# Kernel tuning notes

Measured on AMD Instinct MI355X. Metric: run time of the kernel, lower is better.

## Reference

```python
import jax, jax.numpy as jnp
import numpy as np

N_NODES = 50000
N_EDGES = 800000
D_IN = 128
D_HID = 512
D_OUT = 128


def setup_inputs() -> dict:
    key = jax.random.key(0)
    k1, k2, k3, k4, k5, k6 = jax.random.split(key, 6)
    input_matrix = jax.random.normal(k1, (N_NODES, D_IN), dtype=jnp.float32)
    adjacency_coo_matrix = jax.random.randint(k2, (2, N_EDGES), 0, N_NODES, dtype=jnp.int64)
    # fc net params (torch Linear: y = x @ W.T + b); store W already transposed [D_IN, D_HID]
    lim_fc = 1.0 / np.sqrt(D_IN)
    fc_w = jax.random.uniform(k3, (D_IN, D_HID), dtype=jnp.float32, minval=-lim_fc, maxval=lim_fc)
    fc_b = jax.random.uniform(k4, (D_HID,), dtype=jnp.float32, minval=-lim_fc, maxval=lim_fc)
    # xavier_uniform for [D_IN + D_HID, D_OUT]
    lim_w = np.sqrt(6.0 / (D_IN + D_HID + D_OUT))
    weights_matrix = jax.random.uniform(k5, (D_IN + D_HID, D_OUT), dtype=jnp.float32, minval=-lim_w, maxval=lim_w)
    return {
        "input_matrix": input_matrix,
        "fc_w": fc_w,
        "fc_b": fc_b,
        "weights_matrix": weights_matrix,
        "adjacency_coo_matrix": adjacency_coo_matrix,
    }


def reference(input_matrix, fc_w, fc_b, weights_matrix, adjacency_coo_matrix):
    edge_src, edge_trg = adjacency_coo_matrix[0], adjacency_coo_matrix[1]
    n_nodes = input_matrix.shape[0]
    # gather neighbor features: [E, D_IN]
    neighbors = input_matrix[edge_trg]
    # per-edge MLP + relu: [E, D_HID]
    neighbors_repr = jax.nn.relu(neighbors @ fc_w + fc_b)
    # scatter-max reduce into per-node slots; relu outputs are >= 0, and
    # empty segments map to 0 (matching torch_scatter zero-fill), so clamp at 0
    agg = jax.ops.segment_max(neighbors_repr, edge_src, num_segments=n_nodes)
    agg = jnp.maximum(agg, 0.0)
    concat = jnp.concatenate([input_matrix, agg], axis=1)  # [N, D_IN + D_HID]
    return concat @ weights_matrix  # [N, D_OUT]
```

## Files before the change

kernel.cpp:

```cpp
#include <hip/hip_runtime.h>
#include <hip/hip_bf16.h>

#define N_NODES 50000
#define N_EDGES 800000
#define D_IN 128
#define D_HID 512
#define D_OUT 128
#define CAT_DIM 640
#define CAP 64

typedef __attribute__((ext_vector_type(8))) short short8;
typedef __attribute__((ext_vector_type(4))) float floatx4;

__device__ __forceinline__ unsigned short f2bf(float f) {
    unsigned u = __float_as_uint(f);
    unsigned r = u + 0x7fffu + ((u >> 16) & 1u);
    return (unsigned short)(r >> 16);
}

__device__ __forceinline__ void cvt8(const float* __restrict__ src, unsigned short* o) {
    float4 v0 = *(const float4*)src;
    float4 v1 = *(const float4*)(src + 4);
    o[0] = f2bf(v0.x); o[1] = f2bf(v0.y); o[2] = f2bf(v0.z); o[3] = f2bf(v0.w);
    o[4] = f2bf(v1.x); o[5] = f2bf(v1.y); o[6] = f2bf(v1.z); o[7] = f2bf(v1.w);
}


#define P0_FCW_BLOCKS 256
#define P0_W2_BLOCKS  320
#define P0_DEG_BLOCKS 196
#define P0_BLOCKS (P0_FCW_BLOCKS + P0_W2_BLOCKS + P0_DEG_BLOCKS)

__global__ void prep0_kernel(const float* __restrict__ fcW, const float* __restrict__ Wm,
                             unsigned short* __restrict__ fcwT,
                             unsigned short* __restrict__ WT,
                             int* __restrict__ deg) {
    int b = blockIdx.x, tid = threadIdx.x;
    if (b < P0_FCW_BLOCKS) {
        int idx = b * 256 + tid;
        int k = idx >> 9;
        int n = idx & (D_HID - 1);
        fcwT[n * D_IN + k] = f2bf(fcW[idx]);
        return;
    }
    b -= P0_FCW_BLOCKS;
    if (b < P0_W2_BLOCKS) {
        int idx = b * 256 + tid;
        int k = idx >> 7;
        int n = idx & (D_OUT - 1);
        WT[n * CAT_DIM + k] = f2bf(Wm[idx]);
        return;
    }
    b -= P0_W2_BLOCKS;
    int idx = b * 256 + tid;
    if (idx < N_NODES) deg[idx] = 0;
}


__device__ __forceinline__ void hist_edges(const int* __restrict__ adj, int s, int e0,
                                           int* __restrict__ deg, int* __restrict__ edge_list) {
    int src0, src1, trg0, trg1;
    if (s == 2) {
        int4 vs = *(const int4*)(adj + 2 * (size_t)e0);
        int4 vt = *(const int4*)(adj + 2 * ((size_t)N_EDGES + e0));
        src0 = vs.x; src1 = vs.z;
        trg0 = vt.x; trg1 = vt.z;
    } else {
        int2 vs = *(const int2*)(adj + e0);
        int2 vt = *(const int2*)(adj + N_EDGES + e0);
        src0 = vs.x; src1 = vs.y;
        trg0 = vt.x; trg1 = vt.y;
    }
    int p0 = atomicAdd(&deg[src0], 1);
    if (p0 < CAP) edge_list[src0 * CAP + p0] = trg0;
    int p1 = atomicAdd(&deg[src1], 1);
    if (p1 < CAP) edge_list[src1 * CAP + p1] = trg1;
}


#define HIST_BLOCKS 1563
#define GEMM_MT      782
#define G1_PAD 8

__global__ __launch_bounds__(256)
void mid_kernel(const int* __restrict__ adj,
                int* __restrict__ deg, int* __restrict__ edge_list,
                const float* __restrict__ X,
                const unsigned short* __restrict__ fcwT,
                const float* __restrict__ fcb,
                unsigned short* __restrict__ F) {
    int tid = threadIdx.x;
    if (blockIdx.x < HIST_BLOCKS) {
        int v = adj[2 * (tid & 63) + 1];
        int s = (__ballot(v != 0) == 0ULL) ? 2 : 1;
        int e0 = (blockIdx.x * 256 + tid) * 2;
        if (e0 < N_EDGES) hist_edges(adj, s, e0, deg, edge_list);
        return;
    }
    __shared__ unsigned short As[64][D_IN + G1_PAD];
    __shared__ unsigned short Bs[64][D_IN + G1_PAD];
    int lane = tid & 63, w = tid >> 6;
    int bm = (blockIdx.x - HIST_BLOCKS) * 64;
    {
        int r = tid >> 4;
        int c = (tid & 15) * 8;
        #pragma unroll
        for (int p = 0; p < 4; ++p) {
            int row = r + p * 16;
            int gr = bm + row;
            unsigned short o[8] = {0, 0, 0, 0, 0, 0, 0, 0};
            if (gr < N_NODES) cvt8(X + (size_t)gr * D_IN + c, o);
            *(uint4*)(&As[row][c]) = *(const uint4*)o;
        }
    }
    int wm = (w >> 1) * 32, wn = (w & 1) * 32;
    int q = lane >> 4, l16 = lane & 15;
    for (int nc = 0; nc < 8; ++nc) {
        {
            int r = tid >> 4;
            int c = (tid & 15) * 8;
            #pragma unroll
            for (int p = 0; p < 4; ++p) {
                int row = r + p * 16;
                *(uint4*)(&Bs[row][c]) =
                    *(const uint4*)(fcwT + (size_t)(nc * 64 + row) * D_IN + c);
            }
        }
        __syncthreads();
        floatx4 acc[2][2] = {};
        #pragma unroll
        for (int ks = 0; ks < 4; ++ks) {
            short8 af[2], bf[2];
            #pragma unroll
            for (int mi = 0; mi < 2; ++mi)
                af[mi] = *(const short8*)(&As[wm + mi * 16 + l16][ks * 32 + q * 8]);
            #pragma unroll
            for (int ni = 0; ni < 2; ++ni)
                bf[ni] = *(const short8*)(&Bs[wn + ni * 16 + l16][ks * 32 + q * 8]);
            #pragma unroll
            for (int mi = 0; mi < 2; ++mi)
                #pragma unroll
                for (int ni = 0; ni < 2; ++ni)
                    acc[mi][ni] = __builtin_amdgcn_mfma_f32_16x16x32_bf16(af[mi], bf[ni], acc[mi][ni], 0, 0, 0);
        }
        #pragma unroll
        for (int mi = 0; mi < 2; ++mi)
            #pragma unroll
            for (int ni = 0; ni < 2; ++ni)
                #pragma unroll
                for (int r = 0; r < 4; ++r) {
                    int row = bm + wm + mi * 16 + q * 4 + r;
                    int col = nc * 64 + wn + ni * 16 + l16;
                    if (row < N_NODES) {
                        float v = fmaxf(acc[mi][ni][r] + fcb[col], 0.0f);
                        F[(size_t)row * D_HID + col] = f2bf(v);
                    }
                }
        __syncthreads();
    }
}


__device__ __forceinline__ void fmax_bf16x8(float* acc, const uint4& p) {
    const unsigned* a = (const unsigned*)&p;
    #pragma unroll
    for (int j = 0; j < 4; ++j) {
        unsigned u = a[j];
        acc[2 * j]     = fmaxf(acc[2 * j],     __uint_as_float(u << 16));
        acc[2 * j + 1] = fmaxf(acc[2 * j + 1], __uint_as_float(u & 0xffff0000u));
    }
}

__global__ __launch_bounds__(256)
void aggregate_kernel(const unsigned short* __restrict__ F,
                      const int* __restrict__ deg,
                      const int* __restrict__ edge_list,
                      unsigned short* __restrict__ agg) {
    int gw = (blockIdx.x * 256 + threadIdx.x) >> 6;
    if (gw >= N_NODES) return;
    int lane = threadIdx.x & 63;
    int d = deg[gw];
    d = d < CAP ? d : CAP;
    const int* el = edge_list + gw * CAP;
    float acc[8] = {0.f, 0.f, 0.f, 0.f, 0.f, 0.f, 0.f, 0.f};
    int i = 0;
    for (; i + 2 <= d; i += 2) {
        int t0 = el[i], t1 = el[i + 1];
        uint4 p0 = *(const uint4*)(F + (size_t)t0 * D_HID + lane * 8);
        uint4 p1 = *(const uint4*)(F + (size_t)t1 * D_HID + lane * 8);
        fmax_bf16x8(acc, p0);
        fmax_bf16x8(acc, p1);
    }
    if (i < d) {
        uint4 p0 = *(const uint4*)(F + (size_t)el[i] * D_HID + lane * 8);
        fmax_bf16x8(acc, p0);
    }
    unsigned out[4];
    #pragma unroll
    for (int j = 0; j < 4; ++j) {
        unsigned lo = __float_as_uint(acc[2 * j]) >> 16;
        unsigned hi = __float_as_uint(acc[2 * j + 1]) & 0xffff0000u;
        out[j] = lo | hi;
    }
    *(uint4*)(agg + (size_t)gw * D_HID + lane * 8) = *(uint4*)out;
}


#define GPAD 8

__global__ __launch_bounds__(256)
void gemm2_kernel(const float* __restrict__ X,
                  const unsigned short* __restrict__ agg,
                  const unsigned short* __restrict__ WT,
                  float* __restrict__ out) {
    __shared__ unsigned short As[64][64 + GPAD];
    __shared__ unsigned short Bs[128][64 + GPAD];
    int tid = threadIdx.x;
    int lane = tid & 63, w = tid >> 6;
    int wm = (w >> 1) * 32, wn = (w & 1) * 64;
    int q = lane >> 4, l16 = lane & 15;
    int bm = blockIdx.x * 64;
    floatx4 acc[2][4] = {};
    int ra = tid >> 2;
    int ca = (tid & 3) * 8;
    int rb = tid >> 1;
    int cb = (tid & 1) * 8;

    for (int k0 = 0; k0 < CAT_DIM; k0 += 64) {
        {
            int gr = bm + ra;
            #pragma unroll
            for (int p = 0; p < 2; ++p) {
                int col = k0 + ca + p * 32;
                unsigned short o[8] = {0, 0, 0, 0, 0, 0, 0, 0};
                if (gr < N_NODES) {
                    if (col < D_IN) cvt8(X + (size_t)gr * D_IN + col, o);
                    else *(uint4*)o = *(const uint4*)(agg + (size_t)gr * D_HID + (col - D_IN));
                }
                *(uint4*)(&As[ra][ca + p * 32]) = *(const uint4*)o;
            }
        }
        {
            const unsigned short* bp = WT + (size_t)rb * CAT_DIM + k0 + cb;
            #pragma unroll
            for (int p = 0; p < 4; ++p)
                *(uint4*)(&Bs[rb][cb + p * 16]) = *(const uint4*)(bp + p * 16);
        }
        __syncthreads();
        #pragma unroll
        for (int ks = 0; ks < 2; ++ks) {
            short8 af[2], bf[4];
            #pragma unroll
            for (int mi = 0; mi < 2; ++mi)
                af[mi] = *(const short8*)(&As[wm + mi * 16 + l16][ks * 32 + q * 8]);
            #pragma unroll
            for (int ni = 0; ni < 4; ++ni)
                bf[ni] = *(const short8*)(&Bs[wn + ni * 16 + l16][ks * 32 + q * 8]);
            #pragma unroll
            for (int mi = 0; mi < 2; ++mi)
                #pragma unroll
                for (int ni = 0; ni < 4; ++ni)
                    acc[mi][ni] = __builtin_amdgcn_mfma_f32_16x16x32_bf16(af[mi], bf[ni], acc[mi][ni], 0, 0, 0);
        }
        __syncthreads();
    }

    #pragma unroll
    for (int mi = 0; mi < 2; ++mi)
        #pragma unroll
        for (int ni = 0; ni < 4; ++ni)
            #pragma unroll
            for (int r = 0; r < 4; ++r) {
                int row = bm + wm + mi * 16 + q * 4 + r;
                int col = wn + ni * 16 + l16;
                if (row < N_NODES)
                    out[(size_t)row * D_OUT + col] = acc[mi][ni][r];
            }
}


extern "C" void kernel_launch(void* const* d_in, const int* in_sizes, int n_in,
                              void* d_out, int out_size, void* d_ws, size_t ws_size,
                              hipStream_t stream) {
    const float* X    = (const float*)d_in[0];
    const float* fc_w = (const float*)d_in[1];
    const float* fc_b = (const float*)d_in[2];
    const float* Wm   = (const float*)d_in[3];
    const int*   adj  = (const int*)d_in[4];
    float* outp = (float*)d_out;

    char* ws = (char*)d_ws;
    size_t off = 0;
    auto alloc = [&](size_t bytes) -> void* {
        void* p = ws + off;
        off = (off + bytes + 255) & ~(size_t)255;
        return p;
    };
    unsigned short* agg    = (unsigned short*)alloc((size_t)N_NODES * D_HID * 2);
    unsigned short* F      = (unsigned short*)alloc((size_t)N_NODES * D_HID * 2);
    unsigned short* fcwT   = (unsigned short*)alloc((size_t)D_HID * D_IN * 2);
    unsigned short* WT     = (unsigned short*)alloc((size_t)D_OUT * CAT_DIM * 2);
    int* deg       = (int*)alloc((size_t)N_NODES * 4);
    int* edge_list = (int*)alloc((size_t)N_NODES * CAP * 4);

    prep0_kernel<<<P0_BLOCKS, 256, 0, stream>>>(fc_w, Wm, fcwT, WT, deg);
    mid_kernel<<<HIST_BLOCKS + GEMM_MT, 256, 0, stream>>>(adj, deg, edge_list,
                                                          X, fcwT, fc_b, F);
    aggregate_kernel<<<(N_NODES * 64) / 256, 256, 0, stream>>>(F, deg, edge_list, agg);
    gemm2_kernel<<<GEMM_MT, 256, 0, stream>>>(X, agg, WT, outp);
}
```

Baseline: 290.0 us.

## Split GEMM1 into 64x128 output tiles across four times more blocks

The per-node MLP GEMM in mid_kernel previously used one block per 64-row tile, looping over eight 64-column chunks of the hidden dimension. It now assigns one block per 64x128 output tile (4 column tiles per row tile) and splits K=128 into two 64-wide stages, so each warp computes a 32x64 subtile. This raises block count and parallelism and keeps accumulators resident across K, but each block must re-load and re-convert its X rows, so the fp32 X read is repeated four times.

```diff
diff --git a/kernel.cpp b/kernel.cpp
--- a/kernel.cpp
+++ b/kernel.cpp
@@ -80,7 +80,8 @@
 
 #define HIST_BLOCKS 1563
 #define GEMM_MT      782
-#define G1_PAD 8
+#define GEMM1_TILES (GEMM_MT * 4)
+#define GPAD 8
 
 __global__ __launch_bounds__(256)
 void mid_kernel(const int* __restrict__ adj,
@@ -97,67 +98,67 @@
         if (e0 < N_EDGES) hist_edges(adj, s, e0, deg, edge_list);
         return;
     }
-    __shared__ unsigned short As[64][D_IN + G1_PAD];
-    __shared__ unsigned short Bs[64][D_IN + G1_PAD];
+    __shared__ unsigned short As[64][64 + GPAD];
+    __shared__ unsigned short Bs[128][64 + GPAD];
     int lane = tid & 63, w = tid >> 6;
-    int bm = (blockIdx.x - HIST_BLOCKS) * 64;
-    {
-        int r = tid >> 4;
-        int c = (tid & 15) * 8;
+    int tile = blockIdx.x - HIST_BLOCKS;
+    int bm = (tile >> 2) * 64, bn = (tile & 3) * 128;
+    int wm = (w >> 1) * 32, wn = (w & 1) * 64;
+    int q = lane >> 4, l16 = lane & 15;
+    floatx4 acc[2][4] = {};
+    int ra = tid >> 2;
+    int ca = (tid & 3) * 8;
+    int rb = tid >> 1;
+    int cb = (tid & 1) * 8;
+
+    for (int k0 = 0; k0 < D_IN; k0 += 64) {
+        {
+            int gr = bm + ra;
+            #pragma unroll
+            for (int p = 0; p < 2; ++p) {
+                unsigned short o[8] = {0, 0, 0, 0, 0, 0, 0, 0};
+                if (gr < N_NODES) cvt8(X + (size_t)gr * D_IN + k0 + ca + p * 32, o);
+                *(uint4*)(&As[ra][ca + p * 32]) = *(const uint4*)o;
+            }
+        }
+        {
+            const unsigned short* bp = fcwT + (size_t)(bn + rb) * D_IN + k0 + cb;
+            #pragma unroll
+            for (int p = 0; p < 4; ++p)
+                *(uint4*)(&Bs[rb][cb + p * 16]) = *(const uint4*)(bp + p * 16);
+        }
+        __syncthreads();
         #pragma unroll
-        for (int p = 0; p < 4; ++p) {
-            int row = r + p * 16;
-            int gr = bm + row;
-            unsigned short o[8] = {0, 0, 0, 0, 0, 0, 0, 0};
-            if (gr < N_NODES) cvt8(X + (size_t)gr * D_IN + c, o);
-            *(uint4*)(&As[row][c]) = *(const uint4*)o;
-        }
-    }
-    int wm = (w >> 1) * 32, wn = (w & 1) * 32;
-    int q = lane >> 4, l16 = lane & 15;
-    for (int nc = 0; nc < 8; ++nc) {
-        {
-            int r = tid >> 4;
-            int c = (tid & 15) * 8;
-            #pragma unroll
-            for (int p = 0; p < 4; ++p) {
-                int row = r + p * 16;
-                *(uint4*)(&Bs[row][c]) =
-                    *(const uint4*)(fcwT + (size_t)(nc * 64 + row) * D_IN + c);
-            }
-        }
-        __syncthreads();
-        floatx4 acc[2][2] = {};
-        #pragma unroll
-        for (int ks = 0; ks < 4; ++ks) {
-            short8 af[2], bf[2];
+        for (int ks = 0; ks < 2; ++ks) {
+            short8 af[2], bf[4];
             #pragma unroll
             for (int mi = 0; mi < 2; ++mi)
                 af[mi] = *(const short8*)(&As[wm + mi * 16 + l16][ks * 32 + q * 8]);
             #pragma unroll
-            for (int ni = 0; ni < 2; ++ni)
+            for (int ni = 0; ni < 4; ++ni)
                 bf[ni] = *(const short8*)(&Bs[wn + ni * 16 + l16][ks * 32 + q * 8]);
             #pragma unroll
             for (int mi = 0; mi < 2; ++mi)
                 #pragma unroll
-                for (int ni = 0; ni < 2; ++ni)
+                for (int ni = 0; ni < 4; ++ni)
                     acc[mi][ni] = __builtin_amdgcn_mfma_f32_16x16x32_bf16(af[mi], bf[ni], acc[mi][ni], 0, 0, 0);
         }
+        __syncthreads();
+    }
+
+    #pragma unroll
+    for (int mi = 0; mi < 2; ++mi)
         #pragma unroll
-        for (int mi = 0; mi < 2; ++mi)
-            #pragma unroll
-            for (int ni = 0; ni < 2; ++ni)
-                #pragma unroll
-                for (int r = 0; r < 4; ++r) {
-                    int row = bm + wm + mi * 16 + q * 4 + r;
-                    int col = nc * 64 + wn + ni * 16 + l16;
-                    if (row < N_NODES) {
-                        float v = fmaxf(acc[mi][ni][r] + fcb[col], 0.0f);
-                        F[(size_t)row * D_HID + col] = f2bf(v);
-                    }
+        for (int ni = 0; ni < 4; ++ni)
+            #pragma unroll
+            for (int r = 0; r < 4; ++r) {
+                int row = bm + wm + mi * 16 + q * 4 + r;
+                int col = bn + wn + ni * 16 + l16;
+                if (row < N_NODES) {
+                    float v = fmaxf(acc[mi][ni][r] + fcb[col], 0.0f);
+                    F[(size_t)row * D_HID + col] = f2bf(v);
                 }
-        __syncthreads();
-    }
+            }
 }
 
 
@@ -206,8 +207,6 @@
 }
 
 
-#define GPAD 8
-
 __global__ __launch_bounds__(256)
 void gemm2_kernel(const float* __restrict__ X,
                   const unsigned short* __restrict__ agg,
@@ -304,8 +303,8 @@
     int* edge_list = (int*)alloc((size_t)N_NODES * CAP * 4);
 
     prep0_kernel<<<P0_BLOCKS, 256, 0, stream>>>(fc_w, Wm, fcwT, WT, deg);
-    mid_kernel<<<HIST_BLOCKS + GEMM_MT, 256, 0, stream>>>(adj, deg, edge_list,
-                                                          X, fcwT, fc_b, F);
+    mid_kernel<<<HIST_BLOCKS + GEMM1_TILES, 256, 0, stream>>>(adj, deg, edge_list,
+                                                              X, fcwT, fc_b, F);
     aggregate_kernel<<<(N_NODES * 64) / 256, 256, 0, stream>>>(F, deg, edge_list, agg);
     gemm2_kernel<<<GEMM_MT, 256, 0, stream>>>(X, agg, WT, outp);
 }
```

New measurement: 290.3 us. Within noise of the previous version (+0.1%).
